# Kernel optimization log

Measured on AMD Instinct MI355X. Metric: run time of the kernel, lower is better.

The kernel has to match this reference:

```python
import jax, jax.numpy as jnp
import numpy as np

D_MODEL = 1024
DK = 64
N_HEADS = D_MODEL // DK
MASK = True


def setup_inputs() -> dict:
    key = jax.random.key(0)
    ks = jax.random.split(key, 8)
    B, S = 4, 2048
    scale = 1.0 / np.sqrt(D_MODEL)
    return {
        "query_data": jax.random.normal(ks[0], (B, S, D_MODEL), dtype=jnp.float32),
        "key_data": jax.random.normal(ks[1], (B, S, D_MODEL), dtype=jnp.float32),
        "value_data": jax.random.normal(ks[2], (B, S, D_MODEL), dtype=jnp.float32),
        "Wq": jax.random.normal(ks[3], (D_MODEL, D_MODEL), dtype=jnp.float32) * scale,
        "Wk": jax.random.normal(ks[4], (D_MODEL, D_MODEL), dtype=jnp.float32) * scale,
        "Wv": jax.random.normal(ks[5], (D_MODEL, D_MODEL), dtype=jnp.float32) * scale,
        "Wp": jax.random.normal(ks[6], (D_MODEL, D_MODEL), dtype=jnp.float32) * scale,
        "bp": jnp.zeros((D_MODEL,), dtype=jnp.float32),
    }


def reference(query_data, key_data, value_data, Wq, Wk, Wv, Wp, bp):
    B, S, _ = query_data.shape
    # QKV projections, split into heads: (B, H, S, dk)
    def split_heads(x, W):
        return (x @ W.T).reshape(B, -1, N_HEADS, DK).transpose(0, 2, 1, 3)

    q = split_heads(query_data, Wq)
    k = split_heads(key_data, Wk)
    v = split_heads(value_data, Wv)

    scores = jnp.einsum("bhqd,bhkd->bhqk", q, k) / np.sqrt(DK).astype(np.float32)
    if MASK:
        Sq, Sk = scores.shape[-2], scores.shape[-1]
        causal = jnp.triu(jnp.ones((Sq, Sk), dtype=scores.dtype), k=1) * jnp.float32(-1e13)
        scores = scores + causal  # broadcast over (B, H)
    attn = jax.nn.softmax(scores, axis=-1)
    out = jnp.einsum("bhqk,bhkd->bhqd", attn, v)
    out = out.transpose(0, 2, 1, 3).reshape(B, S, D_MODEL)
    # dropout is identity in eval mode
    return out @ Wp.T + bp
```

## Files before the change

kernel.cpp:

```cpp
#include <hip/hip_runtime.h>
#include <hip/hip_bf16.h>
#include <stdint.h>

#define D_MODEL 1024
#define SEQ     2048
#define BATCH   4
#define NH      16
#define DKK     64
#define MROWS   (BATCH * SEQ)

typedef unsigned short u16;
using bf16x8 = __attribute__((ext_vector_type(8))) __bf16;
using f32x4  = __attribute__((ext_vector_type(4))) float;

__device__ __forceinline__ u16 f2bf(float f) {
    union { float f; uint32_t u; } v; v.f = f;
    return (u16)((v.u + 0x7FFFu + ((v.u >> 16) & 1u)) >> 16);
}
__device__ __forceinline__ uint32_t pk2bf(float a, float b) {
    union { __hip_bfloat162 h; uint32_t u; } v;
    v.h = __float22bfloat162_rn(float2{a, b});
    return v.u;
}

__device__ __forceinline__ float fast_exp2(float x) {
    float r; asm("v_exp_f32 %0, %1" : "=v"(r) : "v"(x)); return r;
}
__device__ __forceinline__ float fast_rcp(float x) {
    float r; asm("v_rcp_f32 %0, %1" : "=v"(r) : "v"(x)); return r;
}

__device__ __forceinline__ void gl_lds16(const u16* g, u16* l) {
    __builtin_amdgcn_global_load_lds(
        (__attribute__((address_space(1))) void*)(const_cast<u16*>(g)),
        (__attribute__((address_space(3))) void*)l, 16, 0, 0);
}

__global__ __launch_bounds__(256) void cvt3_kernel(const float* __restrict__ a,
                                                   const float* __restrict__ b,
                                                   const float* __restrict__ c,
                                                   u16* __restrict__ da,
                                                   u16* __restrict__ db,
                                                   u16* __restrict__ dc) {
    const int i = blockIdx.x * 256 + threadIdx.x;
    const int sel = i >> 21, off = i & ((1 << 21) - 1);
    const float* s = (sel == 0) ? a : (sel == 1) ? b : c;
    u16* d = (sel == 0) ? da : (sel == 1) ? db : dc;
    float4 v = ((const float4*)s)[off];
    uint2 o;
    o.x = pk2bf(v.x, v.y); o.y = pk2bf(v.z, v.w);
    ((uint2*)d)[off] = o;
}

__global__ __launch_bounds__(256) void cvt4_kernel(const float* __restrict__ a,
                                                   const float* __restrict__ b,
                                                   const float* __restrict__ c,
                                                   const float* __restrict__ d4,
                                                   u16* __restrict__ da,
                                                   u16* __restrict__ db,
                                                   u16* __restrict__ dc,
                                                   u16* __restrict__ dd) {
    const int i = blockIdx.x * 256 + threadIdx.x;
    const int sel = i >> 18, off = i & ((1 << 18) - 1);
    const float* s = (sel == 0) ? a : (sel == 1) ? b : (sel == 2) ? c : d4;
    u16* d = (sel == 0) ? da : (sel == 1) ? db : (sel == 2) ? dc : dd;
    float4 v = ((const float4*)s)[off];
    uint2 o;
    o.x = pk2bf(v.x, v.y); o.y = pk2bf(v.z, v.w);
    ((uint2*)d)[off] = o;
}

__global__ __launch_bounds__(256, 3) void gemm_qkv(const u16* __restrict__ XQ,
                                                   const u16* __restrict__ XK,
                                                   const u16* __restrict__ XV,
                                                   const u16* __restrict__ WQ,
                                                   const u16* __restrict__ WK,
                                                   const u16* __restrict__ WV,
                                                   u16* __restrict__ Qo,
                                                   u16* __restrict__ Ko,
                                                   u16* __restrict__ Vto) {
    constexpr int K = 1024, N = 1024;
    __shared__ __align__(16) u16 smem[17408];
    u16* ldsA = smem;
    u16* ldsB = smem + 8192;
    u16* ldsT = smem;

    const int which = blockIdx.x >> 9;
    const int inner = blockIdx.x & 511;
    const u16* A  = (which == 0) ? XQ : (which == 1) ? XK : XV;
    const u16* Bw = (which == 0) ? WQ : (which == 1) ? WK : WV;

    const int t = threadIdx.x;
    const int w = t >> 6, lane = t & 63;
    const int quad = lane >> 4, l15 = lane & 15;
    const int x = inner & 7, j = inner >> 3;
    const int bm = x * 8 + (j >> 3), bn = j & 7;
    const int wm = (w >> 1) * 64, wn = (w & 1) * 64;

    const u16* Ab = A  + (size_t)bm * 128 * K;
    const u16* Bb = Bw + (size_t)bn * 128 * K;
    const int srow  = lane >> 2;
    const int scol8 = (lane & 3) * 8;

    f32x4 acc[4][4];
    #pragma unroll
    for (int i = 0; i < 4; ++i)
        #pragma unroll
        for (int jj = 0; jj < 4; ++jj)
            acc[i][jj] = f32x4{0.f, 0.f, 0.f, 0.f};

    #pragma unroll
    for (int i = 0; i < 2; ++i) {
        const int c = w * 2 + i;
        gl_lds16(Ab + (size_t)(c * 16 + srow) * K + scol8, &ldsA[c * 512]);
        gl_lds16(Bb + (size_t)(c * 16 + srow) * K + scol8, &ldsB[c * 512]);
    }

    int cur = 0;
    for (int k0 = 0; k0 < K; k0 += 32) {
        __syncthreads();
        if (k0 + 32 < K) {
            const int nxt = cur ^ 1;
            #pragma unroll
            for (int i = 0; i < 2; ++i) {
                const int c = w * 2 + i;
                gl_lds16(Ab + (size_t)(c * 16 + srow) * K + k0 + 32 + scol8, &ldsA[nxt * 4096 + c * 512]);
                gl_lds16(Bb + (size_t)(c * 16 + srow) * K + k0 + 32 + scol8, &ldsB[nxt * 4096 + c * 512]);
            }
        }

        bf16x8 afr[4], bfr[4];
        #pragma unroll
        for (int i = 0; i < 4; ++i)
            afr[i] = *(const bf16x8*)&ldsA[cur * 4096 + (wm + i * 16 + l15) * 32 + quad * 8];
        #pragma unroll
        for (int jj = 0; jj < 4; ++jj)
            bfr[jj] = *(const bf16x8*)&ldsB[cur * 4096 + (wn + jj * 16 + l15) * 32 + quad * 8];

        #pragma unroll
        for (int i = 0; i < 4; ++i)
            #pragma unroll
            for (int jj = 0; jj < 4; ++jj)
                acc[i][jj] = __builtin_amdgcn_mfma_f32_16x16x32_bf16(afr[i], bfr[jj], acc[i][jj], 0, 0, 0);
        cur ^= 1;
    }

    __syncthreads();

    if (which < 2) {
        u16* outb = which ? Ko : Qo;
        #pragma unroll
        for (int i = 0; i < 4; ++i)
            #pragma unroll
            for (int jj = 0; jj < 4; ++jj)
                #pragma unroll
                for (int r = 0; r < 4; ++r)
                    ldsT[(wm + i * 16 + quad * 4 + r) * 136 + wn + jj * 16 + l15] = f2bf(acc[i][jj][r]);
        __syncthreads();
        const int rr = t >> 1, half = t & 1;
        const u16* srcl = ldsT + rr * 136 + half * 64;
        u16* dstg = outb + (size_t)(bm * 128 + rr) * N + bn * 128 + half * 64;
        #pragma unroll
        for (int k = 0; k < 8; ++k)
            *(uint4*)(dstg + k * 8) = *(const uint4*)(srcl + k * 8);
    } else {
        #pragma unroll
        for (int i = 0; i < 4; ++i)
            #pragma unroll
            for (int jj = 0; jj < 4; ++jj)
                #pragma unroll
                for (int r = 0; r < 4; ++r) {
                    const int row_l = wm + i * 16 + quad * 4 + r;
                    const int col_l = wn + jj * 16 + l15;
                    ldsT[col_l * 136 + row_l] = f2bf(acc[i][jj][r]);
                }
        __syncthreads();
        const int c = t >> 1, half = t & 1;
        const int colg = bn * 128 + c;
        const int hh = colg >> 6, dd = colg & 63;
        const int bb = bm >> 4;
        const int s0 = ((bm * 128) & 2047) + half * 64;
        const u16* srcl = ldsT + c * 136 + half * 64;
        u16* dstg = Vto + (size_t)((bb * NH + hh) * DKK + dd) * SEQ + s0;
        #pragma unroll
        for (int k = 0; k < 8; ++k)
            *(uint4*)(dstg + k * 8) = *(const uint4*)(srcl + k * 8);
    }
}

__global__ __launch_bounds__(256, 3) void gemm_proj(const u16* __restrict__ A,
                                                    const u16* __restrict__ Bw,
                                                    float* __restrict__ outf,
                                                    const float* __restrict__ bias) {
    constexpr int K = 1024, N = 1024;
    __shared__ __align__(16) u16 ldsA[2 * 4096];
    __shared__ __align__(16) u16 ldsB[2 * 4096];

    const int t = threadIdx.x;
    const int w = t >> 6, lane = t & 63;
    const int quad = lane >> 4, l15 = lane & 15;
    const int x = blockIdx.x & 7, j = blockIdx.x >> 3;
    const int bm = x * 8 + ((j & 63) >> 3), bn = j & 7;
    const int wm = (w >> 1) * 64, wn = (w & 1) * 64;

    const u16* Ab = A  + (size_t)bm * 128 * K;
    const u16* Bb = Bw + (size_t)bn * 128 * K;
    const int srow  = lane >> 2;
    const int scol8 = (lane & 3) * 8;

    f32x4 acc[4][4];
    #pragma unroll
    for (int i = 0; i < 4; ++i)
        #pragma unroll
        for (int jj = 0; jj < 4; ++jj)
            acc[i][jj] = f32x4{0.f, 0.f, 0.f, 0.f};

    #pragma unroll
    for (int i = 0; i < 2; ++i) {
        const int c = w * 2 + i;
        gl_lds16(Ab + (size_t)(c * 16 + srow) * K + scol8, &ldsA[c * 512]);
        gl_lds16(Bb + (size_t)(c * 16 + srow) * K + scol8, &ldsB[c * 512]);
    }

    int cur = 0;
    for (int k0 = 0; k0 < K; k0 += 32) {
        __syncthreads();
        if (k0 + 32 < K) {
            const int nxt = cur ^ 1;
            #pragma unroll
            for (int i = 0; i < 2; ++i) {
                const int c = w * 2 + i;
                gl_lds16(Ab + (size_t)(c * 16 + srow) * K + k0 + 32 + scol8, &ldsA[nxt * 4096 + c * 512]);
                gl_lds16(Bb + (size_t)(c * 16 + srow) * K + k0 + 32 + scol8, &ldsB[nxt * 4096 + c * 512]);
            }
        }

        bf16x8 afr[4], bfr[4];
        #pragma unroll
        for (int i = 0; i < 4; ++i)
            afr[i] = *(const bf16x8*)&ldsA[cur * 4096 + (wm + i * 16 + l15) * 32 + quad * 8];
        #pragma unroll
        for (int jj = 0; jj < 4; ++jj)
            bfr[jj] = *(const bf16x8*)&ldsB[cur * 4096 + (wn + jj * 16 + l15) * 32 + quad * 8];

        #pragma unroll
        for (int i = 0; i < 4; ++i)
            #pragma unroll
            for (int jj = 0; jj < 4; ++jj)
                acc[i][jj] = __builtin_amdgcn_mfma_f32_16x16x32_bf16(afr[i], bfr[jj], acc[i][jj], 0, 0, 0);
        cur ^= 1;
    }

    #pragma unroll
    for (int i = 0; i < 4; ++i)
        #pragma unroll
        for (int jj = 0; jj < 4; ++jj)
            #pragma unroll
            for (int r = 0; r < 4; ++r) {
                const int row = bm * 128 + wm + i * 16 + quad * 4 + r;
                const int col = bn * 128 + wn + jj * 16 + l15;
                outf[(size_t)row * N + col] = acc[i][jj][r] + bias[col];
            }
}

__global__ __launch_bounds__(256, 3) void flash_attn(const u16* __restrict__ Qb,
                                                     const u16* __restrict__ Kb,
                                                     const u16* __restrict__ Vt,
                                                     u16* __restrict__ O) {
    __shared__ __align__(16) u16 ldsK[2 * 4096];
    __shared__ __align__(16) u16 ldsV[2 * 4096];
    __shared__ __align__(16) u16 ldsP[4 * 2048];

    const int t = threadIdx.x;
    const int w = t >> 6, lane = t & 63;
    const int quad = lane >> 4, l15 = lane & 15;
    const int bh = blockIdx.x & 63;
    const int qt = 15 - (blockIdx.x >> 6);
    const int b = bh >> 4, h = bh & 15;
    const int q0 = qt * 128;
    const int qw = q0 + w * 32;

    const int srow  = lane >> 2;
    const int scol8 = (lane & 3) * 8;
    const size_t kbase = (size_t)b * SEQ * D_MODEL + h * DKK;
    const size_t vbase = (size_t)(bh * DKK) * SEQ;

    bf16x8 qf[2][2];
    #pragma unroll
    for (int g = 0; g < 2; ++g) {
        const u16* Qrow = Qb + (size_t)(b * SEQ + qw + g * 16 + l15) * D_MODEL + h * DKK;
        qf[g][0] = *(const bf16x8*)(Qrow + quad * 8);
        qf[g][1] = *(const bf16x8*)(Qrow + 32 + quad * 8);
    }

    f32x4 o_acc[2][4];
    #pragma unroll
    for (int g = 0; g < 2; ++g)
        #pragma unroll
        for (int nt = 0; nt < 4; ++nt) o_acc[g][nt] = f32x4{0.f, 0.f, 0.f, 0.f};
    float l_i[2] = {0.f, 0.f};

    const float C2 = 0.18033688f;
    u16* PwS = &ldsP[w * 2048];

    const int ntiles = 2 * qt + 2;

    #pragma unroll
    for (int i = 0; i < 2; ++i) {
        const int e = w * 2 + i, ch = e >> 2, rb = (e & 3) * 16;
        gl_lds16(Kb + kbase + (size_t)(rb + srow) * D_MODEL + ch * 32 + scol8,
                 &ldsK[ch * 2048 + rb * 32]);
        gl_lds16(Vt + vbase + (size_t)(rb + srow) * SEQ + ch * 32 + scol8,
                 &ldsV[ch * 2048 + rb * 32]);
    }

    int cur = 0;
    for (int it = 0; it < ntiles; ++it) {
        const int kb = it * 64;
        __syncthreads();

        if (it + 1 < ntiles) {
            const int nb = kb + 64, nxt = cur ^ 1;
            #pragma unroll
            for (int i = 0; i < 2; ++i) {
                const int e = w * 2 + i, ch = e >> 2, rb = (e & 3) * 16;
                gl_lds16(Kb + kbase + (size_t)(nb + rb + srow) * D_MODEL + ch * 32 + scol8,
                         &ldsK[nxt * 4096 + ch * 2048 + rb * 32]);
                gl_lds16(Vt + vbase + (size_t)(rb + srow) * SEQ + nb + ch * 32 + scol8,
                         &ldsV[nxt * 4096 + ch * 2048 + rb * 32]);
            }
        }

        if (kb <= qw + 31) {
            f32x4 sc[2][4];
            #pragma unroll
            for (int g = 0; g < 2; ++g)
                #pragma unroll
                for (int jt = 0; jt < 4; ++jt) sc[g][jt] = f32x4{0.f, 0.f, 0.f, 0.f};
            #pragma unroll
            for (int ks = 0; ks < 2; ++ks)
                #pragma unroll
                for (int jt = 0; jt < 4; ++jt) {
                    bf16x8 kf = *(const bf16x8*)&ldsK[cur * 4096 + ks * 2048 + (jt * 16 + l15) * 32 + quad * 8];
                    #pragma unroll
                    for (int g = 0; g < 2; ++g)
                        sc[g][jt] = __builtin_amdgcn_mfma_f32_16x16x32_bf16(kf, qf[g][ks], sc[g][jt], 0, 0, 0);
                }

            if (kb + 63 >= qw) {
                #pragma unroll
                for (int g = 0; g < 2; ++g)
                    #pragma unroll
                    for (int jt = 0; jt < 4; ++jt)
                        #pragma unroll
                        for (int r = 0; r < 4; ++r)
                            if (kb + jt * 16 + quad * 4 + r > qw + g * 16 + l15) sc[g][jt][r] = -3.0e38f;
            }

            #pragma unroll
            for (int g = 0; g < 2; ++g) {
                float tsum = 0.f;
                #pragma unroll
                for (int jt = 0; jt < 4; ++jt) {
                    float p[4];
                    #pragma unroll
                    for (int r = 0; r < 4; ++r) {
                        p[r] = fast_exp2(sc[g][jt][r] * C2);
                        tsum += p[r];
                    }
                    const int pos = (4 * jt + quad) ^ l15;
                    uint2 pk;
                    pk.x = pk2bf(p[0], p[1]);
                    pk.y = pk2bf(p[2], p[3]);
                    *(uint2*)&PwS[g * 1024 + l15 * 64 + pos * 4] = pk;
                }
                tsum += __shfl_xor(tsum, 16);
                tsum += __shfl_xor(tsum, 32);
                l_i[g] += tsum;
            }

            asm volatile("s_waitcnt lgkmcnt(0)" ::: "memory");

            #pragma unroll
            for (int ks = 0; ks < 2; ++ks) {
                const int gg = 8 * ks + 2 * quad;
                union { bf16x8 v; uint2 u[2]; } pu[2];
                #pragma unroll
                for (int g = 0; g < 2; ++g) {
                    pu[g].u[0] = *(const uint2*)&PwS[g * 1024 + l15 * 64 + ((gg) ^ l15) * 4];
                    pu[g].u[1] = *(const uint2*)&PwS[g * 1024 + l15 * 64 + ((gg + 1) ^ l15) * 4];
                }
                #pragma unroll
                for (int nt = 0; nt < 4; ++nt) {
                    bf16x8 vf = *(const bf16x8*)&ldsV[cur * 4096 + ks * 2048 + (nt * 16 + l15) * 32 + quad * 8];
                    #pragma unroll
                    for (int g = 0; g < 2; ++g)
                        o_acc[g][nt] = __builtin_amdgcn_mfma_f32_16x16x32_bf16(pu[g].v, vf, o_acc[g][nt], 0, 0, 0);
                }
            }
        }

        cur ^= 1;
    }

    #pragma unroll
    for (int g = 0; g < 2; ++g) {
        const float rli = fast_rcp(l_i[g]);
        float rl[4];
        #pragma unroll
        for (int r = 0; r < 4; ++r)
            rl[r] = __shfl(rli, (lane & 48) | (quad * 4 + r));
        #pragma unroll
        for (int nt = 0; nt < 4; ++nt)
            #pragma unroll
            for (int r = 0; r < 4; ++r) {
                const int qg = qw + g * 16 + quad * 4 + r;
                O[(size_t)(b * SEQ + qg) * D_MODEL + h * DKK + nt * 16 + l15] = f2bf(o_acc[g][nt][r] * rl[r]);
            }
    }
}

extern "C" void kernel_launch(void* const* d_in, const int* in_sizes, int n_in,
                              void* d_out, int out_size, void* d_ws, size_t ws_size,
                              hipStream_t stream) {
    const float* q_in = (const float*)d_in[0];
    const float* k_in = (const float*)d_in[1];
    const float* v_in = (const float*)d_in[2];
    const float* Wq   = (const float*)d_in[3];
    const float* Wk   = (const float*)d_in[4];
    const float* Wv   = (const float*)d_in[5];
    const float* Wp   = (const float*)d_in[6];
    const float* bp   = (const float*)d_in[7];
    float* out = (float*)d_out;

    char* ws = (char*)d_ws;
    u16* XQ  = (u16*)(ws + (size_t)0);
    u16* XK  = (u16*)(ws + ((size_t)16 << 20));
    u16* XV  = (u16*)(ws + ((size_t)32 << 20));
    u16* WQb = (u16*)(ws + ((size_t)48 << 20));
    u16* WKb = (u16*)(ws + ((size_t)50 << 20));
    u16* WVb = (u16*)(ws + ((size_t)52 << 20));
    u16* WPb = (u16*)(ws + ((size_t)54 << 20));
    u16* Qb  = (u16*)(ws + ((size_t)56 << 20));
    u16* Kb  = (u16*)(ws + ((size_t)72 << 20));
    u16* Vtb = (u16*)(ws + ((size_t)88 << 20));

    cvt3_kernel<<<3 * (1 << 21) / 256, 256, 0, stream>>>(q_in, k_in, v_in, XQ, XK, XV);
    cvt4_kernel<<<4 * (1 << 18) / 256, 256, 0, stream>>>(Wq, Wk, Wv, Wp, WQb, WKb, WVb, WPb);

    gemm_qkv<<<1536, 256, 0, stream>>>(XQ, XK, XV, WQb, WKb, WVb, Qb, Kb, Vtb);

    flash_attn<<<BATCH * NH * (SEQ / 128), 256, 0, stream>>>(Qb, Kb, Vtb, XQ);

    gemm_proj<<<512, 256, 0, stream>>>(XQ, WPb, out, bp);
}
```

Measured before the change: 309.4 us.

## Fuse conversions, swizzle QKV epilogue LDS, shrink proj tiles and attention P buffer

Merges the two fp32-to-bf16 conversion kernels into one launch. Replaces the padded LDS transpose in the QKV GEMM epilogue with an XOR swizzle, which shrinks shared memory. The projection GEMM moves to 64-row tiles with twice as many blocks and a higher occupancy bound. In flash attention the per-wave P buffer is halved by processing the two row groups one after another, so the kernel can run four blocks per CU. The cost is extra waitcnt stalls inside the attention loop and lower data reuse per projection tile.

```diff
diff --git a/kernel.cpp b/kernel.cpp
--- a/kernel.cpp
+++ b/kernel.cpp
@@ -36,34 +36,38 @@
         (__attribute__((address_space(3))) void*)l, 16, 0, 0);
 }
 
-__global__ __launch_bounds__(256) void cvt3_kernel(const float* __restrict__ a,
-                                                   const float* __restrict__ b,
-                                                   const float* __restrict__ c,
-                                                   u16* __restrict__ da,
-                                                   u16* __restrict__ db,
-                                                   u16* __restrict__ dc) {
+__device__ __forceinline__ int swz(int o, int n) {
+    const int pos = ((n >> 3) ^ (o & 15)) ^ (((o >> 4) & 1) << 2);
+    return o * 128 + (pos << 3) + (n & 7);
+}
+__device__ __forceinline__ int swzg(int o, int gn) {
+    const int pos = (gn ^ (o & 15)) ^ (((o >> 4) & 1) << 2);
+    return o * 128 + (pos << 3);
+}
+
+__global__ __launch_bounds__(256) void cvt_all(const float* __restrict__ a,
+                                               const float* __restrict__ b,
+                                               const float* __restrict__ c,
+                                               const float* __restrict__ wq,
+                                               const float* __restrict__ wk,
+                                               const float* __restrict__ wv,
+                                               const float* __restrict__ wp,
+                                               u16* __restrict__ da, u16* __restrict__ db,
+                                               u16* __restrict__ dc, u16* __restrict__ dq,
+                                               u16* __restrict__ dk, u16* __restrict__ dv,
+                                               u16* __restrict__ dp) {
     const int i = blockIdx.x * 256 + threadIdx.x;
-    const int sel = i >> 21, off = i & ((1 << 21) - 1);
-    const float* s = (sel == 0) ? a : (sel == 1) ? b : c;
-    u16* d = (sel == 0) ? da : (sel == 1) ? db : dc;
-    float4 v = ((const float4*)s)[off];
-    uint2 o;
-    o.x = pk2bf(v.x, v.y); o.y = pk2bf(v.z, v.w);
-    ((uint2*)d)[off] = o;
-}
-
-__global__ __launch_bounds__(256) void cvt4_kernel(const float* __restrict__ a,
-                                                   const float* __restrict__ b,
-                                                   const float* __restrict__ c,
-                                                   const float* __restrict__ d4,
-                                                   u16* __restrict__ da,
-                                                   u16* __restrict__ db,
-                                                   u16* __restrict__ dc,
-                                                   u16* __restrict__ dd) {
-    const int i = blockIdx.x * 256 + threadIdx.x;
-    const int sel = i >> 18, off = i & ((1 << 18) - 1);
-    const float* s = (sel == 0) ? a : (sel == 1) ? b : (sel == 2) ? c : d4;
-    u16* d = (sel == 0) ? da : (sel == 1) ? db : (sel == 2) ? dc : dd;
+    const float* s; u16* d; int off;
+    if (i < 3 * (1 << 21)) {
+        const int sel = i >> 21; off = i & ((1 << 21) - 1);
+        s = (sel == 0) ? a : (sel == 1) ? b : c;
+        d = (sel == 0) ? da : (sel == 1) ? db : dc;
+    } else {
+        const int j = i - 3 * (1 << 21);
+        const int sel = j >> 18; off = j & ((1 << 18) - 1);
+        s = (sel == 0) ? wq : (sel == 1) ? wk : (sel == 2) ? wv : wp;
+        d = (sel == 0) ? dq : (sel == 1) ? dk : (sel == 2) ? dv : dp;
+    }
     float4 v = ((const float4*)s)[off];
     uint2 o;
     o.x = pk2bf(v.x, v.y); o.y = pk2bf(v.z, v.w);
@@ -80,7 +84,7 @@
                                                    u16* __restrict__ Ko,
                                                    u16* __restrict__ Vto) {
     constexpr int K = 1024, N = 1024;
-    __shared__ __align__(16) u16 smem[17408];
+    __shared__ __align__(16) u16 smem[16384];
     u16* ldsA = smem;
     u16* ldsB = smem + 8192;
     u16* ldsT = smem;
@@ -155,70 +159,69 @@
             for (int jj = 0; jj < 4; ++jj)
                 #pragma unroll
                 for (int r = 0; r < 4; ++r)
-                    ldsT[(wm + i * 16 + quad * 4 + r) * 136 + wn + jj * 16 + l15] = f2bf(acc[i][jj][r]);
+                    ldsT[swz(wm + i * 16 + quad * 4 + r, wn + jj * 16 + l15)] = f2bf(acc[i][jj][r]);
         __syncthreads();
         const int rr = t >> 1, half = t & 1;
-        const u16* srcl = ldsT + rr * 136 + half * 64;
-        u16* dstg = outb + (size_t)(bm * 128 + rr) * N + bn * 128 + half * 64;
-        #pragma unroll
-        for (int k = 0; k < 8; ++k)
-            *(uint4*)(dstg + k * 8) = *(const uint4*)(srcl + k * 8);
+        u16* dstg = outb + (size_t)(bm * 128 + rr) * N + bn * 128;
+        #pragma unroll
+        for (int k = 0; k < 8; ++k) {
+            const int gn = half * 8 + k;
+            *(uint4*)(dstg + gn * 8) = *(const uint4*)&ldsT[swzg(rr, gn)];
+        }
     } else {
         #pragma unroll
         for (int i = 0; i < 4; ++i)
             #pragma unroll
             for (int jj = 0; jj < 4; ++jj)
                 #pragma unroll
-                for (int r = 0; r < 4; ++r) {
-                    const int row_l = wm + i * 16 + quad * 4 + r;
-                    const int col_l = wn + jj * 16 + l15;
-                    ldsT[col_l * 136 + row_l] = f2bf(acc[i][jj][r]);
-                }
+                for (int r = 0; r < 4; ++r)
+                    ldsT[swz(wn + jj * 16 + l15, wm + i * 16 + quad * 4 + r)] = f2bf(acc[i][jj][r]);
         __syncthreads();
         const int c = t >> 1, half = t & 1;
         const int colg = bn * 128 + c;
         const int hh = colg >> 6, dd = colg & 63;
         const int bb = bm >> 4;
-        const int s0 = ((bm * 128) & 2047) + half * 64;
-        const u16* srcl = ldsT + c * 136 + half * 64;
+        const int s0 = (bm * 128) & 2047;
         u16* dstg = Vto + (size_t)((bb * NH + hh) * DKK + dd) * SEQ + s0;
         #pragma unroll
-        for (int k = 0; k < 8; ++k)
-            *(uint4*)(dstg + k * 8) = *(const uint4*)(srcl + k * 8);
-    }
-}
-
-__global__ __launch_bounds__(256, 3) void gemm_proj(const u16* __restrict__ A,
+        for (int k = 0; k < 8; ++k) {
+            const int gn = half * 8 + k;
+            *(uint4*)(dstg + gn * 8) = *(const uint4*)&ldsT[swzg(c, gn)];
+        }
+    }
+}
+
+__global__ __launch_bounds__(256, 4) void gemm_proj(const u16* __restrict__ A,
                                                     const u16* __restrict__ Bw,
                                                     float* __restrict__ outf,
                                                     const float* __restrict__ bias) {
     constexpr int K = 1024, N = 1024;
-    __shared__ __align__(16) u16 ldsA[2 * 4096];
+    __shared__ __align__(16) u16 ldsA[2 * 2048];
     __shared__ __align__(16) u16 ldsB[2 * 4096];
 
     const int t = threadIdx.x;
     const int w = t >> 6, lane = t & 63;
     const int quad = lane >> 4, l15 = lane & 15;
     const int x = blockIdx.x & 7, j = blockIdx.x >> 3;
-    const int bm = x * 8 + ((j & 63) >> 3), bn = j & 7;
-    const int wm = (w >> 1) * 64, wn = (w & 1) * 64;
-
-    const u16* Ab = A  + (size_t)bm * 128 * K;
+    const int bm = x * 16 + (j >> 3), bn = j & 7;
+    const int wm = (w >> 1) * 32, wn = (w & 1) * 64;
+
+    const u16* Ab = A  + (size_t)bm * 64 * K;
     const u16* Bb = Bw + (size_t)bn * 128 * K;
     const int srow  = lane >> 2;
     const int scol8 = (lane & 3) * 8;
 
-    f32x4 acc[4][4];
-    #pragma unroll
-    for (int i = 0; i < 4; ++i)
+    f32x4 acc[2][4];
+    #pragma unroll
+    for (int i = 0; i < 2; ++i)
         #pragma unroll
         for (int jj = 0; jj < 4; ++jj)
             acc[i][jj] = f32x4{0.f, 0.f, 0.f, 0.f};
 
+    gl_lds16(Ab + (size_t)(w * 16 + srow) * K + scol8, &ldsA[w * 512]);
     #pragma unroll
     for (int i = 0; i < 2; ++i) {
         const int c = w * 2 + i;
-        gl_lds16(Ab + (size_t)(c * 16 + srow) * K + scol8, &ldsA[c * 512]);
         gl_lds16(Bb + (size_t)(c * 16 + srow) * K + scol8, &ldsB[c * 512]);
     }
 
@@ -227,24 +230,24 @@
         __syncthreads();
         if (k0 + 32 < K) {
             const int nxt = cur ^ 1;
+            gl_lds16(Ab + (size_t)(w * 16 + srow) * K + k0 + 32 + scol8, &ldsA[nxt * 2048 + w * 512]);
             #pragma unroll
             for (int i = 0; i < 2; ++i) {
                 const int c = w * 2 + i;
-                gl_lds16(Ab + (size_t)(c * 16 + srow) * K + k0 + 32 + scol8, &ldsA[nxt * 4096 + c * 512]);
                 gl_lds16(Bb + (size_t)(c * 16 + srow) * K + k0 + 32 + scol8, &ldsB[nxt * 4096 + c * 512]);
             }
         }
 
-        bf16x8 afr[4], bfr[4];
-        #pragma unroll
-        for (int i = 0; i < 4; ++i)
-            afr[i] = *(const bf16x8*)&ldsA[cur * 4096 + (wm + i * 16 + l15) * 32 + quad * 8];
+        bf16x8 afr[2], bfr[4];
+        #pragma unroll
+        for (int i = 0; i < 2; ++i)
+            afr[i] = *(const bf16x8*)&ldsA[cur * 2048 + (wm + i * 16 + l15) * 32 + quad * 8];
         #pragma unroll
         for (int jj = 0; jj < 4; ++jj)
             bfr[jj] = *(const bf16x8*)&ldsB[cur * 4096 + (wn + jj * 16 + l15) * 32 + quad * 8];
 
         #pragma unroll
-        for (int i = 0; i < 4; ++i)
+        for (int i = 0; i < 2; ++i)
             #pragma unroll
             for (int jj = 0; jj < 4; ++jj)
                 acc[i][jj] = __builtin_amdgcn_mfma_f32_16x16x32_bf16(afr[i], bfr[jj], acc[i][jj], 0, 0, 0);
@@ -252,24 +255,24 @@
     }
 
     #pragma unroll
-    for (int i = 0; i < 4; ++i)
+    for (int i = 0; i < 2; ++i)
         #pragma unroll
         for (int jj = 0; jj < 4; ++jj)
             #pragma unroll
             for (int r = 0; r < 4; ++r) {
-                const int row = bm * 128 + wm + i * 16 + quad * 4 + r;
+                const int row = bm * 64 + wm + i * 16 + quad * 4 + r;
                 const int col = bn * 128 + wn + jj * 16 + l15;
                 outf[(size_t)row * N + col] = acc[i][jj][r] + bias[col];
             }
 }
 
-__global__ __launch_bounds__(256, 3) void flash_attn(const u16* __restrict__ Qb,
+__global__ __launch_bounds__(256, 4) void flash_attn(const u16* __restrict__ Qb,
                                                      const u16* __restrict__ Kb,
                                                      const u16* __restrict__ Vt,
                                                      u16* __restrict__ O) {
     __shared__ __align__(16) u16 ldsK[2 * 4096];
     __shared__ __align__(16) u16 ldsV[2 * 4096];
-    __shared__ __align__(16) u16 ldsP[4 * 2048];
+    __shared__ __align__(16) u16 ldsP[4 * 1024];
 
     const int t = threadIdx.x;
     const int w = t >> 6, lane = t & 63;
@@ -301,7 +304,7 @@
     float l_i[2] = {0.f, 0.f};
 
     const float C2 = 0.18033688f;
-    u16* PwS = &ldsP[w * 2048];
+    u16* PwS = &ldsP[w * 1024];
 
     const int ntiles = 2 * qt + 2;
 
@@ -372,30 +375,25 @@
                     uint2 pk;
                     pk.x = pk2bf(p[0], p[1]);
                     pk.y = pk2bf(p[2], p[3]);
-                    *(uint2*)&PwS[g * 1024 + l15 * 64 + pos * 4] = pk;
+                    *(uint2*)&PwS[l15 * 64 + pos * 4] = pk;
                 }
                 tsum += __shfl_xor(tsum, 16);
                 tsum += __shfl_xor(tsum, 32);
                 l_i[g] += tsum;
-            }
-
-            asm volatile("s_waitcnt lgkmcnt(0)" ::: "memory");
-
-            #pragma unroll
-            for (int ks = 0; ks < 2; ++ks) {
-                const int gg = 8 * ks + 2 * quad;
-                union { bf16x8 v; uint2 u[2]; } pu[2];
-                #pragma unroll
-                for (int g = 0; g < 2; ++g) {
-                    pu[g].u[0] = *(const uint2*)&PwS[g * 1024 + l15 * 64 + ((gg) ^ l15) * 4];
-                    pu[g].u[1] = *(const uint2*)&PwS[g * 1024 + l15 * 64 + ((gg + 1) ^ l15) * 4];
-                }
-                #pragma unroll
-                for (int nt = 0; nt < 4; ++nt) {
-                    bf16x8 vf = *(const bf16x8*)&ldsV[cur * 4096 + ks * 2048 + (nt * 16 + l15) * 32 + quad * 8];
+
+                asm volatile("s_waitcnt lgkmcnt(0)" ::: "memory");
+
+                #pragma unroll
+                for (int ks = 0; ks < 2; ++ks) {
+                    const int gg = 8 * ks + 2 * quad;
+                    union { bf16x8 v; uint2 u[2]; } pu;
+                    pu.u[0] = *(const uint2*)&PwS[l15 * 64 + ((gg) ^ l15) * 4];
+                    pu.u[1] = *(const uint2*)&PwS[l15 * 64 + ((gg + 1) ^ l15) * 4];
                     #pragma unroll
-                    for (int g = 0; g < 2; ++g)
-                        o_acc[g][nt] = __builtin_amdgcn_mfma_f32_16x16x32_bf16(pu[g].v, vf, o_acc[g][nt], 0, 0, 0);
+                    for (int nt = 0; nt < 4; ++nt) {
+                        bf16x8 vf = *(const bf16x8*)&ldsV[cur * 4096 + ks * 2048 + (nt * 16 + l15) * 32 + quad * 8];
+                        o_acc[g][nt] = __builtin_amdgcn_mfma_f32_16x16x32_bf16(pu.v, vf, o_acc[g][nt], 0, 0, 0);
+                    }
                 }
             }
         }
@@ -445,12 +443,13 @@
     u16* Kb  = (u16*)(ws + ((size_t)72 << 20));
     u16* Vtb = (u16*)(ws + ((size_t)88 << 20));
 
-    cvt3_kernel<<<3 * (1 << 21) / 256, 256, 0, stream>>>(q_in, k_in, v_in, XQ, XK, XV);
-    cvt4_kernel<<<4 * (1 << 18) / 256, 256, 0, stream>>>(Wq, Wk, Wv, Wp, WQb, WKb, WVb, WPb);
+    const int n4 = 3 * (1 << 21) + 4 * (1 << 18);
+    cvt_all<<<n4 / 256, 256, 0, stream>>>(q_in, k_in, v_in, Wq, Wk, Wv, Wp,
+                                          XQ, XK, XV, WQb, WKb, WVb, WPb);
 
     gemm_qkv<<<1536, 256, 0, stream>>>(XQ, XK, XV, WQb, WKb, WVb, Qb, Kb, Vtb);
 
     flash_attn<<<BATCH * NH * (SEQ / 128), 256, 0, stream>>>(Qb, Kb, Vtb, XQ);
 
-    gemm_proj<<<512, 256, 0, stream>>>(XQ, WPb, out, bp);
-}
+    gemm_proj<<<1024, 256, 0, stream>>>(XQ, WPb, out, bp);
+}
```

Result: slower. 327.5 us (+5.9%).
